# Kernel tuning notes

Measured on AMD Instinct MI355X. Metric: run time of the kernel, lower is better.

## Reference

```python
import jax, jax.numpy as jnp
import numpy as np

NEG_INF = -9e15  # matches torch's -9000000000000000.0 fill for masked entries
LEAKY_SLOPE = 0.2


def setup_inputs() -> dict:
    key = jax.random.key(0)
    k1, k2, k3 = jax.random.split(key, 3)
    H, N, D = 4, 4096, 256
    x = jax.random.normal(k1, (H, N, D), dtype=jnp.float32)
    adj = jax.random.randint(k2, (N, N), 0, 2, dtype=jnp.int32)
    # per-head learned attention pattern (xavier-init dense [N,N] in the original)
    att_pattern = jax.random.normal(k3, (H, N, N), dtype=jnp.float32)
    return {"x": x, "adj": adj, "att_pattern": att_pattern,
            "is_val": 0, "epoch": 1, "layer_position": 0}


def reference(x, adj, att_pattern, is_val, epoch, layer_position):
    # x: [H, N, D], adj: [N, N], att_pattern: [H, N, N]
    # leaky_relu on the learned pattern, mask by adjacency, row softmax
    score = jax.nn.leaky_relu(att_pattern, negative_slope=LEAKY_SLOPE)
    score = jnp.where(adj[None, :, :] > 0, score, NEG_INF)
    ratio = jax.nn.softmax(score, axis=-1)  # [H, N, N]
    # dropout is identity in eval/reference mode
    out = jnp.einsum('hnm,hmd->hnd', ratio, x)  # [H, N, D]
    return out
```

## Files before the change

kernel.cpp:

```cpp
#include <hip/hip_runtime.h>

#define NHEAD 4
#define NNODE 4096
#define DIM 256
#define ROWS 64
#define CT 64
#define NT (NNODE / CT)
#define NEGV (-9e15f)

typedef float        f32x4  __attribute__((ext_vector_type(4)));
typedef int          i32x4  __attribute__((ext_vector_type(4)));
typedef unsigned int u32x2  __attribute__((ext_vector_type(2)));
typedef unsigned int u32x4  __attribute__((ext_vector_type(4)));
typedef short        bf16x8 __attribute__((ext_vector_type(8)));
typedef float        f32x16 __attribute__((ext_vector_type(16)));

__device__ __forceinline__ unsigned int f2bf(float f) {
  unsigned int u = __float_as_uint(f);
  u += 0x7fffu + ((u >> 16) & 1u);
  return u >> 16;
}

__global__ __launch_bounds__(256) void prep_all(const float* __restrict__ xg,
                                                const int* __restrict__ adj,
                                                unsigned short* __restrict__ xF,
                                                unsigned short* __restrict__ bits16) {
  const int blk = blockIdx.x;
  const int t = threadIdx.x;
  if (blk < 4096) {
    const int row = blk;
    const int* ap = adj + (size_t)row * NNODE + t * 16;
    const i32x4 j0 = *(const i32x4*)(ap);
    const i32x4 j1 = *(const i32x4*)(ap + 4);
    const i32x4 j2 = *(const i32x4*)(ap + 8);
    const i32x4 j3 = *(const i32x4*)(ap + 12);
    unsigned int m = 0;
#pragma unroll
    for (int k = 0; k < 4; ++k) {
      m |= (j0[k] > 0 ? 1u : 0u) << k;
      m |= (j1[k] > 0 ? 1u : 0u) << (4 + k);
      m |= (j2[k] > 0 ? 1u : 0u) << (8 + k);
      m |= (j3[k] > 0 ? 1u : 0u) << (12 + k);
    }
    bits16[(size_t)row * 256 + t] = (unsigned short)m;
  } else {
    __shared__ unsigned short tile[64 * 260];
    const int b = blk - 4096;
    const int h = b >> 6;
    const int it = b & 63;
    const int n = t >> 2;
    const int dsg = (t & 3) << 6;
    const float* src = xg + ((size_t)h * NNODE + (it << 6) + n) * DIM + dsg;
#pragma unroll
    for (int j = 0; j < 16; ++j) {
      const f32x4 v = *(const f32x4*)(src + 4 * j);
      u32x2 w;
      w[0] = f2bf(v[0]) | (f2bf(v[1]) << 16);
      w[1] = f2bf(v[2]) | (f2bf(v[3]) << 16);
      *(u32x2*)&tile[n * 260 + dsg + 4 * j] = w;
    }
    __syncthreads();
    const int d = t;
    unsigned short* ob = xF + ((size_t)((h << 6) + it) * 2048 + d) * 8;
#pragma unroll
    for (int ks = 0; ks < 4; ++ks)
#pragma unroll
      for (int lh = 0; lh < 2; ++lh) {
        bf16x8 val;
#pragma unroll
        for (int j = 0; j < 8; ++j) val[j] = (short)tile[(ks * 16 + lh * 8 + j) * 260 + d];
        *(bf16x8*)(ob + (size_t)(ks * 2 + lh) * 256 * 8) = val;
      }
  }
}

__global__ __launch_bounds__(1024, 4) void gat_v8(
    const unsigned short* __restrict__ xF, const unsigned int* __restrict__ abits,
    const float* __restrict__ att, float* __restrict__ outg) {
  __shared__ unsigned short p_lds[2][8 * 64 * 8];
  __shared__ float red_lds[8 * 8 * 64 * 4];
  __shared__ float l_lds[ROWS];

  const int t = threadIdx.x;
  const int lane = t & 63;
  const int flat = blockIdx.x;
  const int xcd = flat & 7;
  const int h   = xcd >> 1;
  const int rb  = ((xcd & 1) << 5) | (flat >> 3);
  const int r0  = rb * ROWS;

  const int sr  = t >> 4;
  const int c4  = (t & 15) << 2;
  const float* attb = att + ((size_t)h * NNODE + r0 + sr) * NNODE + c4;
  const unsigned int* ab = abits + (size_t)(r0 + sr) * 128 + (c4 >> 5);
  const int bsh = c4 & 31;
  const int ws_  = c4 >> 3;
  const int pwoff = ws_ * 512 + ((sr ^ ws_) << 3) + (c4 & 7);

  const int wv   = t >> 6;
  const int kh   = wv >> 3;
  const int d0   = (wv & 7) << 5;
  const int lhi  = lane >> 5;
  const int lcol = lane & 31;
  const int s0 = kh * 4 + lhi;
  const int s1 = kh * 4 + 2 + lhi;
  const int aoff00 = s0 * 512 + ((lcol ^ s0) << 3);
  const int aoff01 = s1 * 512 + ((lcol ^ s1) << 3);
  const int aoff10 = s0 * 512 + (((32 + lcol) ^ s0) << 3);
  const int aoff11 = s1 * 512 + (((32 + lcol) ^ s1) << 3);
  const unsigned short* xfb = xF + (size_t)h * NT * 16384 + kh * 8192
                                 + lhi * 2048 + (size_t)(d0 + lcol) * 8;

  f32x16 acc0 = {0.f};
  f32x16 acc1 = {0.f};
  float psum = 0.f;

  bf16x8 xf0 = *(const bf16x8*)(xfb);
  bf16x8 xf1 = *(const bf16x8*)(xfb + 4096);
  f32x4 a0 = __builtin_nontemporal_load((const f32x4*)attb);
  f32x4 a1 = __builtin_nontemporal_load((const f32x4*)(attb + CT));
  unsigned int w0 = ab[0], w1 = ab[2];

  int buf = 0;
  for (int it = 0; it < NT; ++it) {
    const int itn = (it + 1) & (NT - 1);
    const unsigned short* xfi = xfb + (size_t)itn * 16384;
    const bf16x8 nx0 = *(const bf16x8*)(xfi);
    const bf16x8 nx1 = *(const bf16x8*)(xfi + 4096);

    const int it2 = (it + 2) & (NT - 1);
    const f32x4 a2 = __builtin_nontemporal_load((const f32x4*)(attb + it2 * CT));
    const unsigned int w2 = ab[it2 << 1];

    float e0, e1, e2, e3;
    {
      float s0v = a0[0], s1v = a0[1], s2v = a0[2], s3v = a0[3];
      s0v = fmaxf(s0v, 0.2f * s0v); s1v = fmaxf(s1v, 0.2f * s1v);
      s2v = fmaxf(s2v, 0.2f * s2v); s3v = fmaxf(s3v, 0.2f * s3v);
      s0v = ((w0 >> (bsh + 0)) & 1u) ? s0v : NEGV;
      s1v = ((w0 >> (bsh + 1)) & 1u) ? s1v : NEGV;
      s2v = ((w0 >> (bsh + 2)) & 1u) ? s2v : NEGV;
      s3v = ((w0 >> (bsh + 3)) & 1u) ? s3v : NEGV;
      e0 = __expf(s0v); e1 = __expf(s1v); e2 = __expf(s2v); e3 = __expf(s3v);
      psum += (e0 + e1) + (e2 + e3);
    }
    u32x2 pk;
    pk[0] = f2bf(e0) | (f2bf(e1) << 16);
    pk[1] = f2bf(e2) | (f2bf(e3) << 16);
    *(u32x2*)&p_lds[buf][pwoff] = pk;

    asm volatile("s_waitcnt lgkmcnt(0)" ::: "memory");
    __builtin_amdgcn_s_barrier();

    const unsigned short* pb = p_lds[buf];
    const bf16x8 A00 = *(const bf16x8*)&pb[aoff00];
    const bf16x8 A01 = *(const bf16x8*)&pb[aoff01];
    const bf16x8 A10 = *(const bf16x8*)&pb[aoff10];
    const bf16x8 A11 = *(const bf16x8*)&pb[aoff11];
    __builtin_amdgcn_s_setprio(1);
    acc0 = __builtin_amdgcn_mfma_f32_32x32x16_bf16(A00, xf0, acc0, 0, 0, 0);
    acc0 = __builtin_amdgcn_mfma_f32_32x32x16_bf16(A01, xf1, acc0, 0, 0, 0);
    acc1 = __builtin_amdgcn_mfma_f32_32x32x16_bf16(A10, xf0, acc1, 0, 0, 0);
    acc1 = __builtin_amdgcn_mfma_f32_32x32x16_bf16(A11, xf1, acc1, 0, 0, 0);
    __builtin_amdgcn_s_setprio(0);

    a0 = a1; a1 = a2; w0 = w1; w1 = w2;
    xf0 = nx0; xf1 = nx1;
    buf ^= 1;
  }

  float l = psum;
  l += __shfl_xor(l, 1);
  l += __shfl_xor(l, 2);
  l += __shfl_xor(l, 4);
  l += __shfl_xor(l, 8);
  if ((t & 15) == 0) l_lds[sr] = l;
  if (kh == 1) {
    float* rbase = &red_lds[(size_t)(wv & 7) * 2048 + lane * 4];
#pragma unroll
    for (int j = 0; j < 4; ++j) {
      f32x4 v = {acc0[4 * j], acc0[4 * j + 1], acc0[4 * j + 2], acc0[4 * j + 3]};
      *(f32x4*)(rbase + (size_t)j * 256) = v;
    }
#pragma unroll
    for (int j = 0; j < 4; ++j) {
      f32x4 v = {acc1[4 * j], acc1[4 * j + 1], acc1[4 * j + 2], acc1[4 * j + 3]};
      *(f32x4*)(rbase + (size_t)(j + 4) * 256) = v;
    }
  }
  __syncthreads();
  if (kh == 0) {
    const float* rbase = &red_lds[(size_t)wv * 2048 + lane * 4];
#pragma unroll
    for (int j = 0; j < 4; ++j) {
      const f32x4 v = *(const f32x4*)(rbase + (size_t)j * 256);
      acc0[4 * j] += v[0]; acc0[4 * j + 1] += v[1];
      acc0[4 * j + 2] += v[2]; acc0[4 * j + 3] += v[3];
    }
#pragma unroll
    for (int j = 0; j < 4; ++j) {
      const f32x4 v = *(const f32x4*)(rbase + (size_t)(j + 4) * 256);
      acc1[4 * j] += v[0]; acc1[4 * j + 1] += v[1];
      acc1[4 * j + 2] += v[2]; acc1[4 * j + 3] += v[3];
    }
    float* outb = outg + ((size_t)h * NNODE + r0) * DIM + d0 + lcol;
#pragma unroll
    for (int q = 0; q < 4; ++q) {
      const int rbase0 = q * 8 + lhi * 4;
      const f32x4 lv0 = *(const f32x4*)&l_lds[rbase0];
      const f32x4 lv1 = *(const f32x4*)&l_lds[32 + rbase0];
#pragma unroll
      for (int i = 0; i < 4; ++i) {
        __builtin_nontemporal_store(acc0[q * 4 + i] / lv0[i],
                                    outb + (size_t)(rbase0 + i) * DIM);
        __builtin_nontemporal_store(acc1[q * 4 + i] / lv1[i],
                                    outb + (size_t)(32 + rbase0 + i) * DIM);
      }
    }
  }
}

__global__ __launch_bounds__(512, 4) void gat_fused(
    const float* __restrict__ xg, const int* __restrict__ adj,
    const float* __restrict__ att, float* __restrict__ outg) {
  __shared__ __align__(16) unsigned short p_l[64 * 64];
  __shared__ __align__(16) unsigned short xT_l[DIM * 64];
  __shared__ __align__(16) float fac_l[64];
  __shared__ __align__(16) float ll_l[64];
  const int t = threadIdx.x;
  const int lane = t & 63;
  const int flat = blockIdx.x;
  const int xcd  = flat & 7;
  const int h    = xcd >> 1;
  const int rb   = ((xcd & 1) << 5) | (flat >> 3);
  const int r0   = rb * 64;
  const int srow = t >> 3;
  const int sm0  = (t & 7) << 3;
  const float* attb = att + ((size_t)h * NNODE + (r0 + srow)) * NNODE + sm0;
  const int*   adjb = adj + (size_t)(r0 + srow) * NNODE + sm0;
  const int xm0 = (t >> 5) << 2;
  const int xd0 = (t & 31) << 2;
  const float* xb_h = xg + (size_t)h * NNODE * DIM;
  const int wv   = t >> 6;
  const int d0   = wv << 5;
  const int lhi  = lane >> 5;
  const int lcol = lane & 31;
  f32x16 acc0 = {0.f};
  f32x16 acc1 = {0.f};
  float m_run = -__builtin_inff();
  float l_run = 0.f;
  for (int it = 0; it < 64; ++it) {
    const int c0 = it * 64;
    {
      const f32x4 A0 = __builtin_nontemporal_load((const f32x4*)(attb + c0));
      const f32x4 A1 = __builtin_nontemporal_load((const f32x4*)(attb + c0) + 1);
      const i32x4 j0 = *((const i32x4*)(adjb + c0));
      const i32x4 j1 = *((const i32x4*)(adjb + c0) + 1);
      float sv[8];
      int   av[8];
#pragma unroll
      for (int k = 0; k < 4; ++k) { sv[k] = A0[k]; sv[4 + k] = A1[k]; av[k] = j0[k]; av[4 + k] = j1[k]; }
#pragma unroll
      for (int k = 0; k < 8; ++k) {
        float s = sv[k];
        s = s > 0.f ? s : 0.2f * s;
        sv[k] = (av[k] > 0) ? s : NEGV;
      }
      float tmax = sv[0];
#pragma unroll
      for (int k = 1; k < 8; ++k) tmax = fmaxf(tmax, sv[k]);
      tmax = fmaxf(tmax, __shfl_xor(tmax, 1));
      tmax = fmaxf(tmax, __shfl_xor(tmax, 2));
      tmax = fmaxf(tmax, __shfl_xor(tmax, 4));
      const float m_new = fmaxf(m_run, tmax);
      float ps = 0.f;
#pragma unroll
      for (int k = 0; k < 8; ++k) { sv[k] = __expf(sv[k] - m_new); ps += sv[k]; }
      ps += __shfl_xor(ps, 1);
      ps += __shfl_xor(ps, 2);
      ps += __shfl_xor(ps, 4);
      const float fac = __expf(m_run - m_new);
      l_run = l_run * fac + ps;
      m_run = m_new;
      if ((t & 7) == 0) fac_l[srow] = fac;
      u32x4 pk;
      pk[0] = f2bf(sv[0]) | (f2bf(sv[1]) << 16);
      pk[1] = f2bf(sv[2]) | (f2bf(sv[3]) << 16);
      pk[2] = f2bf(sv[4]) | (f2bf(sv[5]) << 16);
      pk[3] = f2bf(sv[6]) | (f2bf(sv[7]) << 16);
      *(u32x4*)&p_l[srow * 64 + (sm0 ^ ((srow & 7) << 3))] = pk;
    }
    {
      const float* xb = xb_h + (size_t)(c0 + xm0) * DIM;
#pragma unroll
      for (int hh2 = 0; hh2 < 2; ++hh2) {
        const int dbase = xd0 + hh2 * 128;
        const f32x4 r0v = *(const f32x4*)(xb + dbase);
        const f32x4 r1v = *(const f32x4*)(xb + DIM + dbase);
        const f32x4 r2v = *(const f32x4*)(xb + 2 * DIM + dbase);
        const f32x4 r3v = *(const f32x4*)(xb + 3 * DIM + dbase);
#pragma unroll
        for (int j = 0; j < 4; ++j) {
          const int d = dbase + j;
          u32x2 wds;
          wds[0] = f2bf(r0v[j]) | (f2bf(r1v[j]) << 16);
          wds[1] = f2bf(r2v[j]) | (f2bf(r3v[j]) << 16);
          *(u32x2*)&xT_l[d * 64 + (xm0 ^ (((d >> 2) & 7) << 3))] = wds;
        }
      }
    }
    __syncthreads();
    {
#pragma unroll
      for (int q = 0; q < 4; ++q) {
        const f32x4 fa = *(const f32x4*)&fac_l[q * 8 + lhi * 4];
        const f32x4 fb = *(const f32x4*)&fac_l[32 + q * 8 + lhi * 4];
#pragma unroll
        for (int i = 0; i < 4; ++i) { acc0[q * 4 + i] *= fa[i]; acc1[q * 4 + i] *= fb[i]; }
      }
#pragma unroll
      for (int ks = 0; ks < 4; ++ks) {
        const int mk = ks * 16 + lhi * 8;
        const bf16x8 afA = *(const bf16x8*)&p_l[lcol * 64 + (mk ^ ((lcol & 7) << 3))];
        const bf16x8 afB = *(const bf16x8*)&p_l[(32 + lcol) * 64 + (mk ^ ((lcol & 7) << 3))];
        const int dd = d0 + lcol;
        const bf16x8 bfr = *(const bf16x8*)&xT_l[dd * 64 + (mk ^ (((dd >> 2) & 7) << 3))];
        acc0 = __builtin_amdgcn_mfma_f32_32x32x16_bf16(afA, bfr, acc0, 0, 0, 0);
        acc1 = __builtin_amdgcn_mfma_f32_32x32x16_bf16(afB, bfr, acc1, 0, 0, 0);
      }
    }
    __syncthreads();
  }
  if ((t & 7) == 0) ll_l[srow] = l_run;
  __syncthreads();
  float* outb = outg + (size_t)h * NNODE * DIM + (size_t)r0 * DIM + d0 + lcol;
#pragma unroll
  for (int q = 0; q < 4; ++q) {
    const f32x4 la = *(const f32x4*)&ll_l[q * 8 + lhi * 4];
    const f32x4 lb = *(const f32x4*)&ll_l[32 + q * 8 + lhi * 4];
    const int rbase = q * 8 + lhi * 4;
#pragma unroll
    for (int i = 0; i < 4; ++i) {
      __builtin_nontemporal_store(acc0[q * 4 + i] / la[i], outb + (size_t)(rbase + i) * DIM);
      __builtin_nontemporal_store(acc1[q * 4 + i] / lb[i], outb + (size_t)(32 + rbase + i) * DIM);
    }
  }
}

extern "C" void kernel_launch(void* const* d_in, const int* in_sizes, int n_in,
                              void* d_out, int out_size, void* d_ws, size_t ws_size,
                              hipStream_t stream) {
  const float* xg  = (const float*)d_in[0];
  const int*   adj = (const int*)d_in[1];
  const float* att = (const float*)d_in[2];
  float*       outg = (float*)d_out;
  const size_t xf_bytes = (size_t)NHEAD * DIM * NNODE * 2;
  const size_t ab_bytes = (size_t)NNODE * 128 * 4;
  if (ws_size >= xf_bytes + ab_bytes) {
    unsigned short* xF    = (unsigned short*)d_ws;
    unsigned int*   abits = (unsigned int*)((char*)d_ws + xf_bytes);
    prep_all<<<dim3(4096 + 256), dim3(256), 0, stream>>>(xg, adj, xF,
                                                         (unsigned short*)abits);
    gat_v8<<<dim3(256), dim3(1024), 0, stream>>>(xF, abits, att, outg);
  } else {
    gat_fused<<<dim3(256), dim3(512), 0, stream>>>(xg, adj, att, outg);
  }
}
```

Measured before the change: 106.5 us.

## Split attention K dimension across two blocks and reduce partials in separate kernel

New measurement: 144.2 us. 1.35x slower.

```diff
diff --git a/kernel.cpp b/kernel.cpp
--- a/kernel.cpp
+++ b/kernel.cpp
@@ -3,9 +3,6 @@
 #define NHEAD 4
 #define NNODE 4096
 #define DIM 256
-#define ROWS 64
-#define CT 64
-#define NT (NNODE / CT)
 #define NEGV (-9e15f)
 
 typedef float        f32x4  __attribute__((ext_vector_type(4)));
@@ -74,21 +71,177 @@
   }
 }
 
+__global__ __launch_bounds__(512, 4) void gat_v9(
+    const unsigned short* __restrict__ xF, const unsigned int* __restrict__ abits,
+    const float* __restrict__ att, float* __restrict__ part,
+    float* __restrict__ lpart) {
+  __shared__ unsigned short p_lds[2][8 * 64 * 8];
+
+  const int t = threadIdx.x;
+  const int lane = t & 63;
+  const int flat = blockIdx.x;
+  const int xcd  = flat & 7;
+  const int h    = xcd >> 1;
+  const int kspl = (flat >> 3) & 1;
+  const int rb   = ((xcd & 1) << 5) | (flat >> 4);
+  const int r0   = rb * 64;
+  const int band = h * 64 + rb;
+
+  const int sr = t >> 3;
+  const int c8 = (t & 7) << 3;
+  const float* attb = att + ((size_t)h * NNODE + r0 + sr) * NNODE + kspl * 2048 + c8;
+  const unsigned int* ab = abits + (size_t)(r0 + sr) * 128 + kspl * 64 + (c8 >> 5);
+  const int bsh = c8 & 31;
+  const int s_w = c8 >> 3;
+  const int pwoff = s_w * 512 + ((sr ^ s_w) << 3);
+
+  const int wv   = t >> 6;
+  const int d0   = wv << 5;
+  const int lhi  = lane >> 5;
+  const int lcol = lane & 31;
+  int aoff0[4], aoff1[4];
+#pragma unroll
+  for (int ks = 0; ks < 4; ++ks) {
+    const int s = ks * 2 + lhi;
+    aoff0[ks] = s * 512 + ((lcol ^ s) << 3);
+    aoff1[ks] = s * 512 + (((32 + lcol) ^ s) << 3);
+  }
+  const unsigned short* xfb = xF + (size_t)(h * 64 + kspl * 32) * 16384
+                                 + lhi * 2048 + (size_t)(d0 + lcol) * 8;
+
+  f32x16 acc0 = {0.f};
+  f32x16 acc1 = {0.f};
+  float psum = 0.f;
+
+  bf16x8 xf0 = *(const bf16x8*)(xfb);
+  bf16x8 xf1 = *(const bf16x8*)(xfb + 4096);
+  bf16x8 xf2 = *(const bf16x8*)(xfb + 8192);
+  bf16x8 xf3 = *(const bf16x8*)(xfb + 12288);
+  f32x4 a0a = __builtin_nontemporal_load((const f32x4*)attb);
+  f32x4 a0b = __builtin_nontemporal_load((const f32x4*)(attb + 4));
+  f32x4 a1a = __builtin_nontemporal_load((const f32x4*)(attb + 64));
+  f32x4 a1b = __builtin_nontemporal_load((const f32x4*)(attb + 68));
+  unsigned int w0 = ab[0], w1 = ab[2];
+
+  int buf = 0;
+  for (int it = 0; it < 32; ++it) {
+    const int itn = (it + 1) & 31;
+    const unsigned short* xfi = xfb + (size_t)itn * 16384;
+    const bf16x8 nx0 = *(const bf16x8*)(xfi);
+    const bf16x8 nx1 = *(const bf16x8*)(xfi + 4096);
+    const bf16x8 nx2 = *(const bf16x8*)(xfi + 8192);
+    const bf16x8 nx3 = *(const bf16x8*)(xfi + 12288);
+
+    const int it2 = (it + 2) & 31;
+    const f32x4 a2a = __builtin_nontemporal_load((const f32x4*)(attb + it2 * 64));
+    const f32x4 a2b = __builtin_nontemporal_load((const f32x4*)(attb + it2 * 64 + 4));
+    const unsigned int w2 = ab[it2 << 1];
+
+    float e[8];
+    {
+      float sv[8];
+#pragma unroll
+      for (int k = 0; k < 4; ++k) { sv[k] = a0a[k]; sv[4 + k] = a0b[k]; }
+#pragma unroll
+      for (int k = 0; k < 8; ++k) {
+        float s = sv[k];
+        s = fmaxf(s, 0.2f * s);
+        s = ((w0 >> (bsh + k)) & 1u) ? s : NEGV;
+        e[k] = __expf(s);
+        psum += e[k];
+      }
+    }
+    u32x4 pk;
+    pk[0] = f2bf(e[0]) | (f2bf(e[1]) << 16);
+    pk[1] = f2bf(e[2]) | (f2bf(e[3]) << 16);
+    pk[2] = f2bf(e[4]) | (f2bf(e[5]) << 16);
+    pk[3] = f2bf(e[6]) | (f2bf(e[7]) << 16);
+    *(u32x4*)&p_lds[buf][pwoff] = pk;
+
+    asm volatile("s_waitcnt lgkmcnt(0)" ::: "memory");
+    __builtin_amdgcn_s_barrier();
+
+    const unsigned short* pb = p_lds[buf];
+    {
+      const bf16x8 A00 = *(const bf16x8*)&pb[aoff0[0]];
+      const bf16x8 A10 = *(const bf16x8*)&pb[aoff1[0]];
+      const bf16x8 A01 = *(const bf16x8*)&pb[aoff0[1]];
+      const bf16x8 A11 = *(const bf16x8*)&pb[aoff1[1]];
+      __builtin_amdgcn_s_setprio(1);
+      acc0 = __builtin_amdgcn_mfma_f32_32x32x16_bf16(A00, xf0, acc0, 0, 0, 0);
+      acc1 = __builtin_amdgcn_mfma_f32_32x32x16_bf16(A10, xf0, acc1, 0, 0, 0);
+      acc0 = __builtin_amdgcn_mfma_f32_32x32x16_bf16(A01, xf1, acc0, 0, 0, 0);
+      acc1 = __builtin_amdgcn_mfma_f32_32x32x16_bf16(A11, xf1, acc1, 0, 0, 0);
+      __builtin_amdgcn_s_setprio(0);
+    }
+    {
+      const bf16x8 A02 = *(const bf16x8*)&pb[aoff0[2]];
+      const bf16x8 A12 = *(const bf16x8*)&pb[aoff1[2]];
+      const bf16x8 A03 = *(const bf16x8*)&pb[aoff0[3]];
+      const bf16x8 A13 = *(const bf16x8*)&pb[aoff1[3]];
+      __builtin_amdgcn_s_setprio(1);
+      acc0 = __builtin_amdgcn_mfma_f32_32x32x16_bf16(A02, xf2, acc0, 0, 0, 0);
+      acc1 = __builtin_amdgcn_mfma_f32_32x32x16_bf16(A12, xf2, acc1, 0, 0, 0);
+      acc0 = __builtin_amdgcn_mfma_f32_32x32x16_bf16(A03, xf3, acc0, 0, 0, 0);
+      acc1 = __builtin_amdgcn_mfma_f32_32x32x16_bf16(A13, xf3, acc1, 0, 0, 0);
+      __builtin_amdgcn_s_setprio(0);
+    }
+
+    a0a = a1a; a0b = a1b; a1a = a2a; a1b = a2b;
+    w0 = w1; w1 = w2;
+    xf0 = nx0; xf1 = nx1; xf2 = nx2; xf3 = nx3;
+    buf ^= 1;
+  }
+
+  float l = psum;
+  l += __shfl_xor(l, 1);
+  l += __shfl_xor(l, 2);
+  l += __shfl_xor(l, 4);
+  if ((t & 7) == 0) lpart[(size_t)(kspl * 256 + band) * 64 + sr] = l;
+
+  float* pout = part + ((size_t)(kspl * 256 + band) * 64) * 256 + d0 + lcol;
+#pragma unroll
+  for (int q = 0; q < 4; ++q) {
+    const int rbase = q * 8 + lhi * 4;
+#pragma unroll
+    for (int i = 0; i < 4; ++i) {
+      __builtin_nontemporal_store(acc0[q * 4 + i], pout + (size_t)(rbase + i) * 256);
+      __builtin_nontemporal_store(acc1[q * 4 + i], pout + (size_t)(32 + rbase + i) * 256);
+    }
+  }
+}
+
+__global__ __launch_bounds__(1024) void reduce_out(const float* __restrict__ part,
+                                                   const float* __restrict__ lpart,
+                                                   float* __restrict__ outg) {
+  const int t = threadIdx.x;
+  const int g = blockIdx.x * 4 + (t >> 8);
+  const int d = t & 255;
+  const int h = g >> 12;
+  const int n = g & 4095;
+  const int band = h * 64 + (n >> 6);
+  const int row = n & 63;
+  const size_t off = ((size_t)band * 64 + row) * 256 + d;
+  const float p0 = part[off];
+  const float p1 = part[(size_t)256 * 64 * 256 + off];
+  const float l  = lpart[(size_t)band * 64 + row] +
+                   lpart[(size_t)256 * 64 + (size_t)band * 64 + row];
+  __builtin_nontemporal_store((p0 + p1) / l, outg + (size_t)g * 256 + d);
+}
+
 __global__ __launch_bounds__(1024, 4) void gat_v8(
     const unsigned short* __restrict__ xF, const unsigned int* __restrict__ abits,
     const float* __restrict__ att, float* __restrict__ outg) {
   __shared__ unsigned short p_lds[2][8 * 64 * 8];
   __shared__ float red_lds[8 * 8 * 64 * 4];
-  __shared__ float l_lds[ROWS];
-
+  __shared__ float l_lds[64];
   const int t = threadIdx.x;
   const int lane = t & 63;
   const int flat = blockIdx.x;
   const int xcd = flat & 7;
   const int h   = xcd >> 1;
   const int rb  = ((xcd & 1) << 5) | (flat >> 3);
-  const int r0  = rb * ROWS;
-
+  const int r0  = rb * 64;
   const int sr  = t >> 4;
   const int c4  = (t & 15) << 2;
   const float* attb = att + ((size_t)h * NNODE + r0 + sr) * NNODE + c4;
@@ -96,7 +249,6 @@
   const int bsh = c4 & 31;
   const int ws_  = c4 >> 3;
   const int pwoff = ws_ * 512 + ((sr ^ ws_) << 3) + (c4 & 7);
-
   const int wv   = t >> 6;
   const int kh   = wv >> 3;
   const int d0   = (wv & 7) << 5;
@@ -108,30 +260,25 @@
   const int aoff01 = s1 * 512 + ((lcol ^ s1) << 3);
   const int aoff10 = s0 * 512 + (((32 + lcol) ^ s0) << 3);
   const int aoff11 = s1 * 512 + (((32 + lcol) ^ s1) << 3);
-  const unsigned short* xfb = xF + (size_t)h * NT * 16384 + kh * 8192
+  const unsigned short* xfb = xF + (size_t)h * 64 * 16384 + kh * 8192
                                  + lhi * 2048 + (size_t)(d0 + lcol) * 8;
-
   f32x16 acc0 = {0.f};
   f32x16 acc1 = {0.f};
   float psum = 0.f;
-
   bf16x8 xf0 = *(const bf16x8*)(xfb);
   bf16x8 xf1 = *(const bf16x8*)(xfb + 4096);
   f32x4 a0 = __builtin_nontemporal_load((const f32x4*)attb);
-  f32x4 a1 = __builtin_nontemporal_load((const f32x4*)(attb + CT));
+  f32x4 a1 = __builtin_nontemporal_load((const f32x4*)(attb + 64));
   unsigned int w0 = ab[0], w1 = ab[2];
-
   int buf = 0;
-  for (int it = 0; it < NT; ++it) {
-    const int itn = (it + 1) & (NT - 1);
+  for (int it = 0; it < 64; ++it) {
+    const int itn = (it + 1) & 63;
     const unsigned short* xfi = xfb + (size_t)itn * 16384;
     const bf16x8 nx0 = *(const bf16x8*)(xfi);
     const bf16x8 nx1 = *(const bf16x8*)(xfi + 4096);
-
-    const int it2 = (it + 2) & (NT - 1);
-    const f32x4 a2 = __builtin_nontemporal_load((const f32x4*)(attb + it2 * CT));
+    const int it2 = (it + 2) & 63;
+    const f32x4 a2 = __builtin_nontemporal_load((const f32x4*)(attb + it2 * 64));
     const unsigned int w2 = ab[it2 << 1];
-
     float e0, e1, e2, e3;
     {
       float s0v = a0[0], s1v = a0[1], s2v = a0[2], s3v = a0[3];
@@ -148,27 +295,21 @@
     pk[0] = f2bf(e0) | (f2bf(e1) << 16);
     pk[1] = f2bf(e2) | (f2bf(e3) << 16);
     *(u32x2*)&p_lds[buf][pwoff] = pk;
-
     asm volatile("s_waitcnt lgkmcnt(0)" ::: "memory");
     __builtin_amdgcn_s_barrier();
-
     const unsigned short* pb = p_lds[buf];
     const bf16x8 A00 = *(const bf16x8*)&pb[aoff00];
     const bf16x8 A01 = *(const bf16x8*)&pb[aoff01];
     const bf16x8 A10 = *(const bf16x8*)&pb[aoff10];
     const bf16x8 A11 = *(const bf16x8*)&pb[aoff11];
-    __builtin_amdgcn_s_setprio(1);
     acc0 = __builtin_amdgcn_mfma_f32_32x32x16_bf16(A00, xf0, acc0, 0, 0, 0);
     acc0 = __builtin_amdgcn_mfma_f32_32x32x16_bf16(A01, xf1, acc0, 0, 0, 0);
     acc1 = __builtin_amdgcn_mfma_f32_32x32x16_bf16(A10, xf0, acc1, 0, 0, 0);
     acc1 = __builtin_amdgcn_mfma_f32_32x32x16_bf16(A11, xf1, acc1, 0, 0, 0);
-    __builtin_amdgcn_s_setprio(0);
-
     a0 = a1; a1 = a2; w0 = w1; w1 = w2;
     xf0 = nx0; xf1 = nx1;
     buf ^= 1;
   }
-
   float l = psum;
   l += __shfl_xor(l, 1);
   l += __shfl_xor(l, 2);
@@ -355,10 +496,20 @@
   const float* att = (const float*)d_in[2];
   float*       outg = (float*)d_out;
   const size_t xf_bytes = (size_t)NHEAD * DIM * NNODE * 2;
-  const size_t ab_bytes = (size_t)NNODE * 128 * 4;
-  if (ws_size >= xf_bytes + ab_bytes) {
-    unsigned short* xF    = (unsigned short*)d_ws;
-    unsigned int*   abits = (unsigned int*)((char*)d_ws + xf_bytes);
+  const size_t ab_off   = xf_bytes;
+  const size_t part_off = 16u * 1024 * 1024;
+  const size_t lp_off   = part_off + (size_t)2 * 256 * 64 * 256 * 4;
+  const size_t need_full = lp_off + (size_t)2 * 256 * 64 * 4;
+  unsigned short* xF    = (unsigned short*)d_ws;
+  unsigned int*   abits = (unsigned int*)((char*)d_ws + ab_off);
+  if (ws_size >= need_full) {
+    float* part  = (float*)((char*)d_ws + part_off);
+    float* lpart = (float*)((char*)d_ws + lp_off);
+    prep_all<<<dim3(4096 + 256), dim3(256), 0, stream>>>(xg, adj, xF,
+                                                         (unsigned short*)abits);
+    gat_v9<<<dim3(512), dim3(512), 0, stream>>>(xF, abits, att, part, lpart);
+    reduce_out<<<dim3(4096), dim3(1024), 0, stream>>>(part, lpart, outg);
+  } else if (ws_size >= xf_bytes + (size_t)NNODE * 128 * 4) {
     prep_all<<<dim3(4096 + 256), dim3(256), 0, stream>>>(xg, adj, xF,
                                                          (unsigned short*)abits);
     gat_v8<<<dim3(256), dim3(1024), 0, stream>>>(xF, abits, att, outg);
```

## Warp-specialize producer and consumer waves with an LDS ring buffer and flags

Applied to the files above, without the earlier changes.

New measurement: 124.7 us. +17.1%, slower.

```diff
diff --git a/kernel.cpp b/kernel.cpp
--- a/kernel.cpp
+++ b/kernel.cpp
@@ -3,9 +3,6 @@
 #define NHEAD 4
 #define NNODE 4096
 #define DIM 256
-#define ROWS 64
-#define CT 64
-#define NT (NNODE / CT)
 #define NEGV (-9e15f)
 
 typedef float        f32x4  __attribute__((ext_vector_type(4)));
@@ -74,135 +71,164 @@
   }
 }
 
-__global__ __launch_bounds__(1024, 4) void gat_v8(
+__global__ __launch_bounds__(1024) void gat_v10(
     const unsigned short* __restrict__ xF, const unsigned int* __restrict__ abits,
     const float* __restrict__ att, float* __restrict__ outg) {
-  __shared__ unsigned short p_lds[2][8 * 64 * 8];
-  __shared__ float red_lds[8 * 8 * 64 * 4];
-  __shared__ float l_lds[ROWS];
+  __shared__ unsigned short ring[8][8 * 64 * 8];
+  __shared__ int flags[64];
+  __shared__ int cdone[64];
+  __shared__ float l_lds[64];
 
   const int t = threadIdx.x;
   const int lane = t & 63;
+  const int wv = t >> 6;
   const int flat = blockIdx.x;
   const int xcd = flat & 7;
   const int h   = xcd >> 1;
   const int rb  = ((xcd & 1) << 5) | (flat >> 3);
-  const int r0  = rb * ROWS;
-
-  const int sr  = t >> 4;
-  const int c4  = (t & 15) << 2;
-  const float* attb = att + ((size_t)h * NNODE + r0 + sr) * NNODE + c4;
-  const unsigned int* ab = abits + (size_t)(r0 + sr) * 128 + (c4 >> 5);
-  const int bsh = c4 & 31;
-  const int ws_  = c4 >> 3;
-  const int pwoff = ws_ * 512 + ((sr ^ ws_) << 3) + (c4 & 7);
-
-  const int wv   = t >> 6;
-  const int kh   = wv >> 3;
-  const int d0   = (wv & 7) << 5;
+  const int r0  = rb * 64;
+
+  if (t < 64) flags[t] = 0;
+  else if (t < 128) cdone[t - 64] = 0;
+  __syncthreads();
+
+  f32x16 acc0 = {0.f};
+  f32x16 acc1 = {0.f};
   const int lhi  = lane >> 5;
   const int lcol = lane & 31;
-  const int s0 = kh * 4 + lhi;
-  const int s1 = kh * 4 + 2 + lhi;
-  const int aoff00 = s0 * 512 + ((lcol ^ s0) << 3);
-  const int aoff01 = s1 * 512 + ((lcol ^ s1) << 3);
-  const int aoff10 = s0 * 512 + (((32 + lcol) ^ s0) << 3);
-  const int aoff11 = s1 * 512 + (((32 + lcol) ^ s1) << 3);
-  const unsigned short* xfb = xF + (size_t)h * NT * 16384 + kh * 8192
-                                 + lhi * 2048 + (size_t)(d0 + lcol) * 8;
-
-  f32x16 acc0 = {0.f};
-  f32x16 acc1 = {0.f};
-  float psum = 0.f;
-
-  bf16x8 xf0 = *(const bf16x8*)(xfb);
-  bf16x8 xf1 = *(const bf16x8*)(xfb + 4096);
-  f32x4 a0 = __builtin_nontemporal_load((const f32x4*)attb);
-  f32x4 a1 = __builtin_nontemporal_load((const f32x4*)(attb + CT));
-  unsigned int w0 = ab[0], w1 = ab[2];
-
-  int buf = 0;
-  for (int it = 0; it < NT; ++it) {
-    const int itn = (it + 1) & (NT - 1);
-    const unsigned short* xfi = xfb + (size_t)itn * 16384;
-    const bf16x8 nx0 = *(const bf16x8*)(xfi);
-    const bf16x8 nx1 = *(const bf16x8*)(xfi + 4096);
-
-    const int it2 = (it + 2) & (NT - 1);
-    const f32x4 a2 = __builtin_nontemporal_load((const f32x4*)(attb + it2 * CT));
-    const unsigned int w2 = ab[it2 << 1];
-
-    float e0, e1, e2, e3;
-    {
-      float s0v = a0[0], s1v = a0[1], s2v = a0[2], s3v = a0[3];
-      s0v = fmaxf(s0v, 0.2f * s0v); s1v = fmaxf(s1v, 0.2f * s1v);
-      s2v = fmaxf(s2v, 0.2f * s2v); s3v = fmaxf(s3v, 0.2f * s3v);
-      s0v = ((w0 >> (bsh + 0)) & 1u) ? s0v : NEGV;
-      s1v = ((w0 >> (bsh + 1)) & 1u) ? s1v : NEGV;
-      s2v = ((w0 >> (bsh + 2)) & 1u) ? s2v : NEGV;
-      s3v = ((w0 >> (bsh + 3)) & 1u) ? s3v : NEGV;
-      e0 = __expf(s0v); e1 = __expf(s1v); e2 = __expf(s2v); e3 = __expf(s3v);
-      psum += (e0 + e1) + (e2 + e3);
-    }
-    u32x2 pk;
-    pk[0] = f2bf(e0) | (f2bf(e1) << 16);
-    pk[1] = f2bf(e2) | (f2bf(e3) << 16);
-    *(u32x2*)&p_lds[buf][pwoff] = pk;
-
-    asm volatile("s_waitcnt lgkmcnt(0)" ::: "memory");
-    __builtin_amdgcn_s_barrier();
-
-    const unsigned short* pb = p_lds[buf];
-    const bf16x8 A00 = *(const bf16x8*)&pb[aoff00];
-    const bf16x8 A01 = *(const bf16x8*)&pb[aoff01];
-    const bf16x8 A10 = *(const bf16x8*)&pb[aoff10];
-    const bf16x8 A11 = *(const bf16x8*)&pb[aoff11];
-    __builtin_amdgcn_s_setprio(1);
-    acc0 = __builtin_amdgcn_mfma_f32_32x32x16_bf16(A00, xf0, acc0, 0, 0, 0);
-    acc0 = __builtin_amdgcn_mfma_f32_32x32x16_bf16(A01, xf1, acc0, 0, 0, 0);
-    acc1 = __builtin_amdgcn_mfma_f32_32x32x16_bf16(A10, xf0, acc1, 0, 0, 0);
-    acc1 = __builtin_amdgcn_mfma_f32_32x32x16_bf16(A11, xf1, acc1, 0, 0, 0);
-    __builtin_amdgcn_s_setprio(0);
-
-    a0 = a1; a1 = a2; w0 = w1; w1 = w2;
-    xf0 = nx0; xf1 = nx1;
-    buf ^= 1;
-  }
-
-  float l = psum;
-  l += __shfl_xor(l, 1);
-  l += __shfl_xor(l, 2);
-  l += __shfl_xor(l, 4);
-  l += __shfl_xor(l, 8);
-  if ((t & 15) == 0) l_lds[sr] = l;
-  if (kh == 1) {
-    float* rbase = &red_lds[(size_t)(wv & 7) * 2048 + lane * 4];
-#pragma unroll
-    for (int j = 0; j < 4; ++j) {
-      f32x4 v = {acc0[4 * j], acc0[4 * j + 1], acc0[4 * j + 2], acc0[4 * j + 3]};
-      *(f32x4*)(rbase + (size_t)j * 256) = v;
-    }
-#pragma unroll
-    for (int j = 0; j < 4; ++j) {
-      f32x4 v = {acc1[4 * j], acc1[4 * j + 1], acc1[4 * j + 2], acc1[4 * j + 3]};
-      *(f32x4*)(rbase + (size_t)(j + 4) * 256) = v;
-    }
-  }
+
+  if (wv < 8) {
+    const int pwv = wv;
+    const int rin = lane >> 3;
+    const int cg  = lane & 7;
+    const int grow = pwv * 8 + rin;
+    const float* attb = att + ((size_t)h * NNODE + r0 + grow) * NNODE + cg * 8;
+    const unsigned int* ab = abits + (size_t)(r0 + grow) * 128 + (cg >> 2);
+    const int bsh = (cg & 3) * 8;
+    const int pwoff = cg * 512 + ((grow ^ cg) << 3);
+
+    float psum = 0.f;
+    f32x4 a0a = __builtin_nontemporal_load((const f32x4*)attb);
+    f32x4 a0b = __builtin_nontemporal_load((const f32x4*)(attb + 4));
+    f32x4 a1a = __builtin_nontemporal_load((const f32x4*)(attb + 64));
+    f32x4 a1b = __builtin_nontemporal_load((const f32x4*)(attb + 68));
+    unsigned int w0 = ab[0], w1 = ab[2];
+
+    for (int it = 0; it < 64; ++it) {
+      const int slot = it & 7;
+      if (it >= 8) {
+        volatile int* cd = (volatile int*)&cdone[slot * 8];
+        const int need = it - 7;
+        for (;;) {
+          int m = cd[0];
+          m = min(m, cd[1]); m = min(m, cd[2]); m = min(m, cd[3]);
+          m = min(m, cd[4]); m = min(m, cd[5]); m = min(m, cd[6]); m = min(m, cd[7]);
+          if (m >= need) break;
+          __builtin_amdgcn_s_sleep(1);
+        }
+      }
+      const int it2 = (it + 2) & 63;
+      const f32x4 a2a = __builtin_nontemporal_load((const f32x4*)(attb + it2 * 64));
+      const f32x4 a2b = __builtin_nontemporal_load((const f32x4*)(attb + it2 * 64 + 4));
+      const unsigned int w2 = ab[it2 * 2];
+
+      float e[8];
+      {
+        float sv[8];
+        sv[0] = a0a[0]; sv[1] = a0a[1]; sv[2] = a0a[2]; sv[3] = a0a[3];
+        sv[4] = a0b[0]; sv[5] = a0b[1]; sv[6] = a0b[2]; sv[7] = a0b[3];
+#pragma unroll
+        for (int k = 0; k < 8; ++k) {
+          float s = sv[k];
+          s = fmaxf(s, 0.2f * s);
+          s = ((w0 >> (bsh + k)) & 1u) ? s : NEGV;
+          e[k] = __expf(s);
+          psum += e[k];
+        }
+      }
+      u32x4 pk;
+      pk[0] = f2bf(e[0]) | (f2bf(e[1]) << 16);
+      pk[1] = f2bf(e[2]) | (f2bf(e[3]) << 16);
+      pk[2] = f2bf(e[4]) | (f2bf(e[5]) << 16);
+      pk[3] = f2bf(e[6]) | (f2bf(e[7]) << 16);
+      *(u32x4*)&ring[slot][pwoff] = pk;
+      asm volatile("s_waitcnt lgkmcnt(0)" ::: "memory");
+      if (lane == 0) flags[slot * 8 + pwv] = it + 1;
+
+      a0a = a1a; a0b = a1b; a1a = a2a; a1b = a2b;
+      w0 = w1; w1 = w2;
+    }
+    psum += __shfl_xor(psum, 1);
+    psum += __shfl_xor(psum, 2);
+    psum += __shfl_xor(psum, 4);
+    if (cg == 0) l_lds[grow] = psum;
+  } else {
+    const int cwv = wv - 8;
+    const int d0 = cwv << 5;
+    int aoff0[4], aoff1[4];
+#pragma unroll
+    for (int ks = 0; ks < 4; ++ks) {
+      const int s = ks * 2 + lhi;
+      aoff0[ks] = s * 512 + ((lcol ^ s) << 3);
+      aoff1[ks] = s * 512 + (((32 + lcol) ^ s) << 3);
+    }
+    const unsigned short* xfb = xF + (size_t)h * 64 * 16384 + lhi * 2048
+                                   + (size_t)(d0 + lcol) * 8;
+    bf16x8 xf0 = *(const bf16x8*)(xfb);
+    bf16x8 xf1 = *(const bf16x8*)(xfb + 4096);
+    bf16x8 xf2 = *(const bf16x8*)(xfb + 8192);
+    bf16x8 xf3 = *(const bf16x8*)(xfb + 12288);
+
+    for (int it = 0; it < 64; ++it) {
+      const int slot = it & 7;
+      const int itn = (it + 1) & 63;
+      const unsigned short* xfi = xfb + (size_t)itn * 16384;
+      const bf16x8 nx0 = *(const bf16x8*)(xfi);
+      const bf16x8 nx1 = *(const bf16x8*)(xfi + 4096);
+      const bf16x8 nx2 = *(const bf16x8*)(xfi + 8192);
+      const bf16x8 nx3 = *(const bf16x8*)(xfi + 12288);
+      {
+        volatile int* vf = (volatile int*)&flags[slot * 8];
+        const int need = it + 1;
+        for (;;) {
+          int m = vf[0];
+          m = min(m, vf[1]); m = min(m, vf[2]); m = min(m, vf[3]);
+          m = min(m, vf[4]); m = min(m, vf[5]); m = min(m, vf[6]); m = min(m, vf[7]);
+          if (m >= need) break;
+          __builtin_amdgcn_s_sleep(1);
+        }
+      }
+      __builtin_amdgcn_sched_barrier(0);
+      const unsigned short* pb = ring[slot];
+      const bf16x8 A00 = *(const bf16x8*)&pb[aoff0[0]];
+      const bf16x8 A10 = *(const bf16x8*)&pb[aoff1[0]];
+      const bf16x8 A01 = *(const bf16x8*)&pb[aoff0[1]];
+      const bf16x8 A11 = *(const bf16x8*)&pb[aoff1[1]];
+      const bf16x8 A02 = *(const bf16x8*)&pb[aoff0[2]];
+      const bf16x8 A12 = *(const bf16x8*)&pb[aoff1[2]];
+      const bf16x8 A03 = *(const bf16x8*)&pb[aoff0[3]];
+      const bf16x8 A13 = *(const bf16x8*)&pb[aoff1[3]];
+      __builtin_amdgcn_s_setprio(1);
+      acc0 = __builtin_amdgcn_mfma_f32_32x32x16_bf16(A00, xf0, acc0, 0, 0, 0);
+      acc1 = __builtin_amdgcn_mfma_f32_32x32x16_bf16(A10, xf0, acc1, 0, 0, 0);
+      acc0 = __builtin_amdgcn_mfma_f32_32x32x16_bf16(A01, xf1, acc0, 0, 0, 0);
+      acc1 = __builtin_amdgcn_mfma_f32_32x32x16_bf16(A11, xf1, acc1, 0, 0, 0);
+      acc0 = __builtin_amdgcn_mfma_f32_32x32x16_bf16(A02, xf2, acc0, 0, 0, 0);
+      acc1 = __builtin_amdgcn_mfma_f32_32x32x16_bf16(A12, xf2, acc1, 0, 0, 0);
+      acc0 = __builtin_amdgcn_mfma_f32_32x32x16_bf16(A03, xf3, acc0, 0, 0, 0);
+      acc1 = __builtin_amdgcn_mfma_f32_32x32x16_bf16(A13, xf3, acc1, 0, 0, 0);
+      __builtin_amdgcn_s_setprio(0);
+      asm volatile("s_waitcnt lgkmcnt(0)" ::: "memory");
+      if (lane == 0) cdone[slot * 8 + cwv] = it + 1;
+      xf0 = nx0; xf1 = nx1; xf2 = nx2; xf3 = nx3;
+    }
+  }
+
   __syncthreads();
-  if (kh == 0) {
-    const float* rbase = &red_lds[(size_t)wv * 2048 + lane * 4];
-#pragma unroll
-    for (int j = 0; j < 4; ++j) {
-      const f32x4 v = *(const f32x4*)(rbase + (size_t)j * 256);
-      acc0[4 * j] += v[0]; acc0[4 * j + 1] += v[1];
-      acc0[4 * j + 2] += v[2]; acc0[4 * j + 3] += v[3];
-    }
-#pragma unroll
-    for (int j = 0; j < 4; ++j) {
-      const f32x4 v = *(const f32x4*)(rbase + (size_t)(j + 4) * 256);
-      acc1[4 * j] += v[0]; acc1[4 * j + 1] += v[1];
-      acc1[4 * j + 2] += v[2]; acc1[4 * j + 3] += v[3];
-    }
+
+  if (wv >= 8) {
+    const int cwv = wv - 8;
+    const int d0 = cwv << 5;
     float* outb = outg + ((size_t)h * NNODE + r0) * DIM + d0 + lcol;
 #pragma unroll
     for (int q = 0; q < 4; ++q) {
@@ -361,7 +387,7 @@
     unsigned int*   abits = (unsigned int*)((char*)d_ws + xf_bytes);
     prep_all<<<dim3(4096 + 256), dim3(256), 0, stream>>>(xg, adj, xF,
                                                          (unsigned short*)abits);
-    gat_v8<<<dim3(256), dim3(1024), 0, stream>>>(xF, abits, att, outg);
+    gat_v10<<<dim3(256), dim3(1024), 0, stream>>>(xF, abits, att, outg);
   } else {
     gat_fused<<<dim3(256), dim3(512), 0, stream>>>(xg, adj, att, outg);
   }
```
